# Kernel optimization log

Measured on AMD Instinct MI355X. Metric: run time of the kernel, lower is better.

## Reference

```python
import jax, jax.numpy as jnp
import numpy as np
import math

N = 10000      # nodes per type
DIN = 64       # input feature dim
HID = 128      # hidden_dim
HEADS = 8      # num_heads
DH = 128       # per-head dim == out_channels (PyG TransformerConv)
INNER = HEADS * DH  # 1024
L = 2          # num_layers
E = 60000      # edges per edge type
FF = 512       # 4*hidden
LN_EPS = 1e-5


def setup_inputs():
    keys = iter(jax.random.split(jax.random.key(0), 80))
    def mk(shape, std=0.05):
        return std * jax.random.normal(next(keys), shape, dtype=jnp.float32)
    inp = {}
    for t in ("job", "mach"):
        inp[f"x_{t}"] = mk((N, DIN), 1.0)
        inp[f"Win_{t}"] = mk((DIN, HID)); inp[f"bin_{t}"] = mk((HID,), 0.01)
        inp[f"pos_{t}"] = mk((N, HID)); inp[f"te_{t}"] = mk((HID,))
        inp[f"lng_{t}"] = 1.0 + mk((L, HID), 0.02); inp[f"lnb_{t}"] = mk((L, HID), 0.02)
        inp[f"W1_{t}"] = mk((L, HID, FF)); inp[f"b1_{t}"] = mk((L, FF), 0.01)
        inp[f"W2_{t}"] = mk((L, FF, HID)); inp[f"b2_{t}"] = mk((L, HID), 0.01)
        inp[f"Wout_{t}"] = mk((HID, HID)); inp[f"bout_{t}"] = mk((HID,), 0.01)
    for et in ("jm", "mj"):
        inp[f"Wq_{et}"] = mk((L, HID, INNER)); inp[f"Wk_{et}"] = mk((L, HID, INNER))
        inp[f"Wv_{et}"] = mk((L, HID, INNER)); inp[f"Ws_{et}"] = mk((L, HID, HID))
        inp[f"Wb_{et}"] = mk((L, 3 * HID, 1))
        inp[f"bq_{et}"] = mk((L, INNER), 0.01); inp[f"bk_{et}"] = mk((L, INNER), 0.01)
        inp[f"bv_{et}"] = mk((L, INNER), 0.01); inp[f"bs_{et}"] = mk((L, HID), 0.01)
        inp[f"ei_{et}"] = jax.random.randint(next(keys), (2, E), 0, N, dtype=jnp.int32)
    return inp


def _layer_norm(x, g, b):
    mu = x.mean(-1, keepdims=True)
    var = ((x - mu) ** 2).mean(-1, keepdims=True)
    return (x - mu) / jnp.sqrt(var + LN_EPS) * g + b


def _tconv(x_src, x_dst, src, dst, Wq, bq, Wk, bk, Wv, bv, Ws, bs, Wb):
    # PyG TransformerConv(heads=HEADS, out_channels=DH, concat=False, beta=True, root_weight=True)
    Nd = x_dst.shape[0]
    q = (x_dst @ Wq + bq).reshape(Nd, HEADS, DH)
    k = (x_src @ Wk + bk).reshape(-1, HEADS, DH)
    v = (x_src @ Wv + bv).reshape(-1, HEADS, DH)
    logits = jnp.einsum('ehd,ehd->eh', q[dst], k[src]) / math.sqrt(DH)  # [E,H]
    # segment softmax over edges grouped by destination node
    m = jax.ops.segment_max(logits, dst, num_segments=Nd)
    m = jnp.where(jnp.isfinite(m), m, 0.0)  # empty segments -> -inf -> 0
    ex = jnp.exp(logits - m[dst])
    den = jax.ops.segment_sum(ex, dst, num_segments=Nd)
    alpha = ex / (den[dst] + 1e-16)
    agg = jax.ops.segment_sum(alpha[:, :, None] * v[src], dst, num_segments=Nd)
    out = agg.mean(axis=1)              # concat=False -> average heads -> [Nd, DH]
    x_r = x_dst @ Ws + bs               # root/skip projection
    beta = jax.nn.sigmoid(jnp.concatenate([out, x_r, out - x_r], axis=-1) @ Wb)  # [Nd,1]
    return beta * x_r + (1.0 - beta) * out


def _ffn_block(h, new, g, b, W1, b1, W2, b2):
    r = _layer_norm(h + new, g, b)
    return r + (jax.nn.gelu(r @ W1 + b1, approximate=False) @ W2 + b2)


def _forward(x_job, Win_job, bin_job, pos_job, te_job, lng_job, lnb_job, W1_job, b1_job, W2_job, b2_job, Wout_job, bout_job, x_mach, Win_mach, bin_mach, pos_mach, te_mach, lng_mach, lnb_mach, W1_mach, b1_mach, W2_mach, b2_mach, Wout_mach, bout_mach, Wq_jm, Wk_jm, Wv_jm, Ws_jm, Wb_jm, bq_jm, bk_jm, bv_jm, bs_jm, ei_jm, Wq_mj, Wk_mj, Wv_mj, Ws_mj, Wb_mj, bq_mj, bk_mj, bv_mj, bs_mj, ei_mj):
    h_j = x_job @ Win_job + bin_job + te_job + pos_job
    h_m = x_mach @ Win_mach + bin_mach + te_mach + pos_mach
    s_jm, d_jm = ei_jm[0], ei_jm[1]  # job -> mach
    s_mj, d_mj = ei_mj[0], ei_mj[1]  # mach -> job
    for l in range(L):
        new_m = _tconv(h_j, h_m, s_jm, d_jm, Wq_jm[l], bq_jm[l], Wk_jm[l], bk_jm[l], Wv_jm[l], bv_jm[l], Ws_jm[l], bs_jm[l], Wb_jm[l])
        new_j = _tconv(h_m, h_j, s_mj, d_mj, Wq_mj[l], bq_mj[l], Wk_mj[l], bk_mj[l], Wv_mj[l], bv_mj[l], Ws_mj[l], bs_mj[l], Wb_mj[l])
        h_j = _ffn_block(h_j, new_j, lng_job[l], lnb_job[l], W1_job[l], b1_job[l], W2_job[l], b2_job[l])
        h_m = _ffn_block(h_m, new_m, lng_mach[l], lnb_mach[l], W1_mach[l], b1_mach[l], W2_mach[l], b2_mach[l])
    return jnp.stack([h_j @ Wout_job + bout_job, h_m @ Wout_mach + bout_mach], axis=0)


def reference(x_job, Win_job, bin_job, pos_job, te_job, lng_job, lnb_job, W1_job, b1_job, W2_job, b2_job, Wout_job, bout_job, x_mach, Win_mach, bin_mach, pos_mach, te_mach, lng_mach, lnb_mach, W1_mach, b1_mach, W2_mach, b2_mach, Wout_mach, bout_mach, Wq_jm, Wk_jm, Wv_jm, Ws_jm, Wb_jm, bq_jm, bk_jm, bv_jm, bs_jm, ei_jm, Wq_mj, Wk_mj, Wv_mj, Ws_mj, Wb_mj, bq_mj, bk_mj, bv_mj, bs_mj, ei_mj):
    return _forward(x_job, Win_job, bin_job, pos_job, te_job, lng_job, lnb_job, W1_job, b1_job, W2_job, b2_job, Wout_job, bout_job, x_mach, Win_mach, bin_mach, pos_mach, te_mach, lng_mach, lnb_mach, W1_mach, b1_mach, W2_mach, b2_mach, Wout_mach, bout_mach, Wq_jm, Wk_jm, Wv_jm, Ws_jm, Wb_jm, bq_jm, bk_jm, bv_jm, bs_jm, ei_jm, Wq_mj, Wk_mj, Wv_mj, Ws_mj, Wb_mj, bq_mj, bk_mj, bv_mj, bs_mj, ei_mj)
```

## Files before the change

### kernel.cpp

```cpp
#include <hip/hip_runtime.h>
#include <hip/hip_bf16.h>

#define NN 10000
#define EE 60000
#define HIDD 128
#define NH 8
#define INNERD 1024
#define FFD 512
#define KVQ 3072
#define KVQS 3200

using u16 = unsigned short;
using u32 = unsigned int;

typedef __bf16 bf16x8 __attribute__((ext_vector_type(8)));
typedef float f32x4 __attribute__((ext_vector_type(4)));

__device__ __forceinline__ float u2f(u32 u) { return __uint_as_float(u << 16); }
__device__ __forceinline__ u16 f2b(float f) {
  u32 x = __float_as_uint(f);
  return (u16)((x + 0x7fffu + ((x >> 16) & 1u)) >> 16);
}
__device__ __forceinline__ float gelu_f(float x) {
  return 0.5f * x * (1.0f + erff(x * 0.70710678118654752f));
}

__global__ void detect_k(const u32* __restrict__ xw, int* __restrict__ flag) {
  if (threadIdx.x == 0 && blockIdx.x == 0) {
    int wild = 0;
    for (int i = 0; i < 256; ++i) {
      float v = u2f(xw[i] & 0xffffu);
      if (!(fabsf(v) < 1e4f)) ++wild;
    }
    *flag = (wild > 16) ? 1 : 0;
  }
}

#define NCVT 30
struct CvtArgs { const void* src[NCVT]; int cnt[NCVT]; int ntot; };

__global__ __launch_bounds__(256) void convert_k(CvtArgs a, const int* __restrict__ flag,
                                                 float* __restrict__ dst) {
  const int i = blockIdx.x * 256 + threadIdx.x;
  if (i >= a.ntot) return;
  int t = 0, off = i;
  while (off >= a.cnt[t]) { off -= a.cnt[t]; ++t; }
  const float v = (*flag) ? ((const float*)a.src[t])[off]
                          : u2f(((const u16*)a.src[t])[off]);
  dst[i] = v;
}

struct TT { const void* s; long off; u16* d; int K; int N; };
struct TTab { TT m[28]; };

__global__ __launch_bounds__(256) void transT_k(TTab tt, const int* __restrict__ flag) {
  const TT m = tt.m[blockIdx.z];
  const int n0 = blockIdx.x * 32, k0 = blockIdx.y * 32;
  if (n0 >= m.N || k0 >= m.K) return;
  __shared__ float tile[32][33];
  const int c = threadIdx.x;
  const int f32in = *flag;
  for (int i = threadIdx.y; i < 32; i += 8) {
    const long gi = m.off + (long)(k0 + i) * m.N + n0 + c;
    tile[i][c] = f32in ? ((const float*)m.s)[gi] : u2f(((const u16*)m.s)[gi]);
  }
  __syncthreads();
  for (int i = threadIdx.y; i < 32; i += 8)
    m.d[(size_t)(n0 + i) * m.K + k0 + c] = f2b(tile[c][i]);
}

__global__ __launch_bounds__(256) void hist_k(const int* __restrict__ ei0,
                                              const int* __restrict__ ei1,
                                              int* __restrict__ hist) {
  const int e = blockIdx.x * 256 + threadIdx.x;
  if (e >= EE) return;
  const int et = blockIdx.y;
  const int* ei = et ? ei1 : ei0;
  atomicAdd(&hist[et * NN + ei[EE + e]], 1);
}

__global__ __launch_bounds__(1024) void scan2_k(const int* __restrict__ hist,
                                                int* __restrict__ rowptr,
                                                int* __restrict__ cursor) {
  const int et = blockIdx.x;
  const int* h = hist + et * NN;
  int* rp = rowptr + et * (NN + 1);
  int* cu = cursor + et * NN;
  __shared__ int wsum[16];
  __shared__ int carrySm;
  const int t = threadIdx.x, lane = t & 63, wid = t >> 6;
  if (t == 0) carrySm = 0;
  __syncthreads();
  for (int base = 0; base < NN; base += 1024) {
    const int idx = base + t;
    const int v = (idx < NN) ? h[idx] : 0;
    int x = v;
#pragma unroll
    for (int off = 1; off < 64; off <<= 1) {
      int y = __shfl_up(x, off);
      if (lane >= off) x += y;
    }
    if (lane == 63) wsum[wid] = x;
    __syncthreads();
    if (wid == 0) {
      int s = (lane < 16) ? wsum[lane] : 0;
#pragma unroll
      for (int off = 1; off < 16; off <<= 1) {
        int y = __shfl_up(s, off);
        if (lane >= off) s += y;
      }
      if (lane < 16) wsum[lane] = s;
    }
    __syncthreads();
    const int waveoff = (wid > 0) ? wsum[wid - 1] : 0;
    const int incl = x + waveoff + carrySm;
    if (idx < NN) { rp[idx] = incl - v; cu[idx] = incl - v; }
    __syncthreads();
    if (t == 1023) carrySm = incl;
    __syncthreads();
  }
  if (t == 0) rp[NN] = carrySm;
}

__global__ __launch_bounds__(256) void scat_k(const int* __restrict__ ei0,
                                              const int* __restrict__ ei1,
                                              int* __restrict__ cursor,
                                              int* __restrict__ srcs) {
  const int e = blockIdx.x * 256 + threadIdx.x;
  if (e >= EE) return;
  const int et = blockIdx.y;
  const int* ei = et ? ei1 : ei0;
  const int s = ei[e], d = ei[EE + e];
  const int pos = atomicAdd(&cursor[et * NN + d], 1);
  srcs[et * EE + pos] = s;
}

__global__ __launch_bounds__(128) void embed2_k(
    const void* __restrict__ x0, const float* __restrict__ Win0,
    const float* __restrict__ bin0, const float* __restrict__ te0,
    const void* __restrict__ pos0, float* __restrict__ h0, u16* __restrict__ h80,
    const void* __restrict__ x1, const float* __restrict__ Win1,
    const float* __restrict__ bin1, const float* __restrict__ te1,
    const void* __restrict__ pos1, float* __restrict__ h1, u16* __restrict__ h81,
    const int* __restrict__ flag) {
  const int ty = blockIdx.y;
  const void* x = ty ? x1 : x0;
  const float* Win = ty ? Win1 : Win0;
  const float* bin = ty ? bin1 : bin0;
  const float* te = ty ? te1 : te0;
  const void* pos = ty ? pos1 : pos0;
  float* h = ty ? h1 : h0;
  u16* h8 = ty ? h81 : h80;
  __shared__ float Ws[64][128];
  __shared__ float xs[16][64];
  const int f32in = *flag;
  const int j = threadIdx.x;
  const int base = blockIdx.x * 16;
  for (int i = 0; i < 64; ++i) Ws[i][j] = Win[i * 128 + j];
  for (int r = 0; r < 8; ++r) {
    int idx = r * 128 + j;
    int row = idx >> 6, k = idx & 63;
    size_t gi = (size_t)(base + row) * 64 + k;
    xs[row][k] = f32in ? ((const float*)x)[gi] : u2f(((const u16*)x)[gi]);
  }
  __syncthreads();
  float bj = bin[j] + te[j];
  for (int row = 0; row < 16; ++row) {
    size_t gi = (size_t)(base + row) * 128 + j;
    float pv = f32in ? ((const float*)pos)[gi] : u2f(((const u16*)pos)[gi]);
    float acc = bj + pv;
#pragma unroll
    for (int k = 0; k < 64; ++k) acc += xs[row][k] * Ws[k][j];
    h[(size_t)(base + row) * 128 + j] = acc;
    h8[(size_t)(base + row) * 128 + j] = f2b(acc);
  }
}

struct MG {
  const u16* A; const u16* WT;
  const float* b0; const float* b1; const float* b2; const float* b3;
  const float* add; float* Cf; u16* Cb;
};

template <int MODE>
__global__ __launch_bounds__(256) void mgemm2_k(MG g0, MG g1, int M, int N, int K) {
  const MG g = blockIdx.z ? g1 : g0;
  __shared__ __align__(16) u16 Asl[128][40];
  __shared__ __align__(16) u16 Bsl[64][40];
  const int t = threadIdx.x;
  const int lane = t & 63, wid = t >> 6;
  const int bm = blockIdx.y * 128, bn = blockIdx.x * 64;
  const int rg = lane >> 4, rr = lane & 15;
  f32x4 acc[2][4];
#pragma unroll
  for (int i = 0; i < 2; ++i)
#pragma unroll
    for (int j = 0; j < 4; ++j) acc[i][j] = (f32x4){0.f, 0.f, 0.f, 0.f};
  const int ar = t >> 1;
  const int ah = (t & 1) << 4;
  const int wr = t >> 2;
  const int wk = (t & 3) << 3;

  for (int k0 = 0; k0 < K; k0 += 32) {
    const int garow = bm + ar;
    uint4 a0 = {0,0,0,0}, a1 = {0,0,0,0};
    if (garow < M) {
      const u16* ap = g.A + (size_t)garow * K + k0 + ah;
      a0 = *reinterpret_cast<const uint4*>(ap);
      a1 = *reinterpret_cast<const uint4*>(ap + 8);
    }
    *reinterpret_cast<uint4*>(&Asl[ar][ah]) = a0;
    *reinterpret_cast<uint4*>(&Asl[ar][ah + 8]) = a1;
    const uint4 bv = *reinterpret_cast<const uint4*>(g.WT + (size_t)(bn + wr) * K + k0 + wk);
    *reinterpret_cast<uint4*>(&Bsl[wr][wk]) = bv;
    __syncthreads();
    bf16x8 af[2], bfr[4];
#pragma unroll
    for (int mi = 0; mi < 2; ++mi)
      af[mi] = *reinterpret_cast<const bf16x8*>(&Asl[wid * 32 + mi * 16 + rr][rg * 8]);
#pragma unroll
    for (int ni = 0; ni < 4; ++ni)
      bfr[ni] = *reinterpret_cast<const bf16x8*>(&Bsl[ni * 16 + rr][rg * 8]);
#pragma unroll
    for (int mi = 0; mi < 2; ++mi)
#pragma unroll
      for (int ni = 0; ni < 4; ++ni)
        acc[mi][ni] = __builtin_amdgcn_mfma_f32_16x16x32_bf16(af[mi], bfr[ni], acc[mi][ni], 0, 0, 0);
    __syncthreads();
  }
#pragma unroll
  for (int mi = 0; mi < 2; ++mi) {
#pragma unroll
    for (int ni = 0; ni < 4; ++ni) {
      const int col = bn + ni * 16 + rr;
      float bcol;
      if (MODE == 2) {
        const int seg = col >> 10;
        const float* bp = (seg == 0) ? g.b0 : ((seg == 1) ? g.b1 : ((seg == 2) ? g.b2 : g.b3));
        bcol = bp[col & 1023];
      } else {
        bcol = g.b0[col];
      }
#pragma unroll
      for (int r = 0; r < 4; ++r) {
        const int row = bm + wid * 32 + mi * 16 + rg * 4 + r;
        if (row >= M) continue;
        float v = acc[mi][ni][r] + bcol;
        if (MODE == 2) {
          if (col < KVQ) g.Cb[(size_t)row * KVQ + col] = f2b(v);
          else           g.Cf[(size_t)row * HIDD + (col - KVQ)] = v;
        } else if (MODE == 3) {
          v = gelu_f(v);
          g.Cb[(size_t)row * N + col] = f2b(v);
        } else {
          v += g.add[(size_t)row * N + col];
          g.Cf[(size_t)row * N + col] = v;
          g.Cb[(size_t)row * N + col] = f2b(v);
        }
      }
    }
  }
}

struct VG {
  const float* A; const float* B; const float* bias;
  float* Cf; u16* Cb;
};

__global__ __launch_bounds__(256) void gemm2_k(VG g0, VG g1, const int* __restrict__ oflag,
                                               int M, int N, int K) {
  const VG g = blockIdx.z ? g1 : g0;
  __shared__ __align__(16) float As[16][64];
  __shared__ __align__(16) float Bs[16][64];
  const int t = threadIdx.x;
  const int tx = t & 15, ty = t >> 4;
  const int bm = blockIdx.y * 64, bn = blockIdx.x * 64;
  float c[4][4] = {{0.f}};
  const int am = t >> 2;
  const int ak = (t & 3) << 2;
  const int bk = t >> 4;
  const int bn4 = (t & 15) << 2;
  for (int k0 = 0; k0 < K; k0 += 16) {
    float4 av = make_float4(0.f, 0.f, 0.f, 0.f);
    const int arow = bm + am;
    if (arow < M) av = *reinterpret_cast<const float4*>(g.A + (size_t)arow * K + k0 + ak);
    As[ak + 0][am] = av.x; As[ak + 1][am] = av.y;
    As[ak + 2][am] = av.z; As[ak + 3][am] = av.w;
    float4 bv = *reinterpret_cast<const float4*>(g.B + (size_t)(k0 + bk) * N + bn + bn4);
    Bs[bk][bn4 + 0] = bv.x; Bs[bk][bn4 + 1] = bv.y;
    Bs[bk][bn4 + 2] = bv.z; Bs[bk][bn4 + 3] = bv.w;
    __syncthreads();
#pragma unroll
    for (int kk = 0; kk < 16; ++kk) {
      float4 a = *reinterpret_cast<const float4*>(&As[kk][ty << 2]);
      float4 b = *reinterpret_cast<const float4*>(&Bs[kk][tx << 2]);
      c[0][0] += a.x * b.x; c[0][1] += a.x * b.y; c[0][2] += a.x * b.z; c[0][3] += a.x * b.w;
      c[1][0] += a.y * b.x; c[1][1] += a.y * b.y; c[1][2] += a.y * b.z; c[1][3] += a.y * b.w;
      c[2][0] += a.z * b.x; c[2][1] += a.z * b.y; c[2][2] += a.z * b.z; c[2][3] += a.z * b.w;
      c[3][0] += a.w * b.x; c[3][1] += a.w * b.y; c[3][2] += a.w * b.z; c[3][3] += a.w * b.w;
    }
    __syncthreads();
  }
  const int f32out = *oflag;
#pragma unroll
  for (int i = 0; i < 4; ++i) {
    const int row = bm + (ty << 2) + i;
    if (row >= M) continue;
#pragma unroll
    for (int j = 0; j < 4; ++j) {
      const int col = bn + (tx << 2) + j;
      float v = c[i][j] + g.bias[col];
      if (f32out) g.Cf[(size_t)row * N + col] = v;
      else        g.Cb[(size_t)row * N + col] = f2b(v);
    }
  }
}

__global__ __launch_bounds__(256) void attn2_k(
    const u16* __restrict__ kvqJ, const u16* __restrict__ kvqM,
    const int* __restrict__ rowptr, const int* __restrict__ srcs,
    float* __restrict__ aggM, float* __restrict__ aggJ) {
  const int et = blockIdx.y;
  const u16* kvqS = et ? kvqM : kvqJ;
  const u16* kvqD = et ? kvqJ : kvqM;
  const int* rp = rowptr + et * (NN + 1);
  const int* sr = srcs + et * EE;
  float* agg = et ? aggJ : aggM;
  const int d = (blockIdx.x * 256 + threadIdx.x) >> 6;
  const int lane = threadIdx.x & 63;
  const u16* qp = kvqD + (size_t)d * KVQ + 2048 + lane * 16;
  uint4 q0 = *reinterpret_cast<const uint4*>(qp);
  uint4 q1 = *reinterpret_cast<const uint4*>(qp + 8);
  float qf[16];
  {
    u32 w[8] = {q0.x, q0.y, q0.z, q0.w, q1.x, q1.y, q1.z, q1.w};
#pragma unroll
    for (int i = 0; i < 8; ++i) { qf[2*i] = u2f(w[i] & 0xffffu); qf[2*i+1] = u2f(w[i] >> 16); }
  }
  float m = -INFINITY, den = 0.f;
  float acc[16];
#pragma unroll
  for (int i = 0; i < 16; ++i) acc[i] = 0.f;
  const int beg = rp[d], end = rp[d + 1];

  auto dot8 = [&](const uint4& a, const uint4& b) -> float {
    float p = 0.f;
    const u32 w[8] = {a.x, a.y, a.z, a.w, b.x, b.y, b.z, b.w};
#pragma unroll
    for (int i = 0; i < 8; ++i) {
      p += qf[2*i] * u2f(w[i] & 0xffffu);
      p += qf[2*i+1] * u2f(w[i] >> 16);
    }
    return p;
  };
  auto update = [&](float part, const uint4& v0w, const uint4& v1w) {
    part += __shfl_xor(part, 1);
    part += __shfl_xor(part, 2);
    part += __shfl_xor(part, 4);
    const float lg = part * 0.088388347648318447f;
    const float nm = fmaxf(m, lg);
    const float cor = __expf(m - nm);
    const float p = __expf(lg - nm);
    den = den * cor + p;
    const u32 w[8] = {v0w.x, v0w.y, v0w.z, v0w.w, v1w.x, v1w.y, v1w.z, v1w.w};
#pragma unroll
    for (int i = 0; i < 8; ++i) {
      acc[2*i]   = acc[2*i]   * cor + p * u2f(w[i] & 0xffffu);
      acc[2*i+1] = acc[2*i+1] * cor + p * u2f(w[i] >> 16);
    }
    m = nm;
  };

  int idx = beg;
  for (; idx + 2 <= end; idx += 2) {
    const int s0 = sr[idx], s1 = sr[idx + 1];
    const u16* kp0 = kvqS + (size_t)s0 * KVQ + lane * 16;
    const u16* kp1 = kvqS + (size_t)s1 * KVQ + lane * 16;
    const uint4 a0 = *reinterpret_cast<const uint4*>(kp0);
    const uint4 a1 = *reinterpret_cast<const uint4*>(kp0 + 8);
    const uint4 av0 = *reinterpret_cast<const uint4*>(kp0 + 1024);
    const uint4 av1 = *reinterpret_cast<const uint4*>(kp0 + 1024 + 8);
    const uint4 b0 = *reinterpret_cast<const uint4*>(kp1);
    const uint4 b1 = *reinterpret_cast<const uint4*>(kp1 + 8);
    const uint4 bv0 = *reinterpret_cast<const uint4*>(kp1 + 1024);
    const uint4 bv1 = *reinterpret_cast<const uint4*>(kp1 + 1024 + 8);
    const float p0 = dot8(a0, a1);
    const float p1 = dot8(b0, b1);
    update(p0, av0, av1);
    update(p1, bv0, bv1);
  }
  if (idx < end) {
    const int s0 = sr[idx];
    const u16* kp0 = kvqS + (size_t)s0 * KVQ + lane * 16;
    const uint4 a0 = *reinterpret_cast<const uint4*>(kp0);
    const uint4 a1 = *reinterpret_cast<const uint4*>(kp0 + 8);
    const uint4 av0 = *reinterpret_cast<const uint4*>(kp0 + 1024);
    const uint4 av1 = *reinterpret_cast<const uint4*>(kp0 + 1024 + 8);
    update(dot8(a0, a1), av0, av1);
  }

  const float inv = 0.125f / (den + 1e-16f);
  float o[16];
#pragma unroll
  for (int i = 0; i < 16; ++i) {
    float tv = acc[i] * inv;
    tv += __shfl_xor(tv, 8);
    tv += __shfl_xor(tv, 16);
    tv += __shfl_xor(tv, 32);
    o[i] = tv;
  }
  if (lane < 8) {
    float* op = agg + (size_t)d * HIDD + lane * 16;
    *reinterpret_cast<float4*>(op + 0)  = make_float4(o[0],  o[1],  o[2],  o[3]);
    *reinterpret_cast<float4*>(op + 4)  = make_float4(o[4],  o[5],  o[6],  o[7]);
    *reinterpret_cast<float4*>(op + 8)  = make_float4(o[8],  o[9],  o[10], o[11]);
    *reinterpret_cast<float4*>(op + 12) = make_float4(o[12], o[13], o[14], o[15]);
  }
}

struct BL {
  const float* agg; const float* xr; const float* Wb;
  const float* h; const float* g; const float* b; float* r; u16* r8;
};

__global__ __launch_bounds__(256) void betaln2_k(BL p0, BL p1) {
  const BL p = blockIdx.y ? p1 : p0;
  const int n = (blockIdx.x * 256 + threadIdx.x) >> 6;
  const int lane = threadIdx.x & 63;
  const float o0 = p.agg[(size_t)n * HIDD + lane], o1 = p.agg[(size_t)n * HIDD + 64 + lane];
  const float x0 = p.xr[(size_t)n * HIDD + lane], x1 = p.xr[(size_t)n * HIDD + 64 + lane];
  float s = o0 * p.Wb[lane] + o1 * p.Wb[64 + lane]
          + x0 * p.Wb[128 + lane] + x1 * p.Wb[192 + lane]
          + (o0 - x0) * p.Wb[256 + lane] + (o1 - x1) * p.Wb[320 + lane];
#pragma unroll
  for (int mask = 1; mask < 64; mask <<= 1) s += __shfl_xor(s, mask);
  const float beta = 1.f / (1.f + expf(-s));
  const float n0 = beta * x0 + (1.f - beta) * o0;
  const float n1 = beta * x1 + (1.f - beta) * o1;
  const float v0 = p.h[(size_t)n * HIDD + lane] + n0;
  const float v1 = p.h[(size_t)n * HIDD + 64 + lane] + n1;
  float sm = v0 + v1;
#pragma unroll
  for (int mask = 1; mask < 64; mask <<= 1) sm += __shfl_xor(sm, mask);
  const float mu = sm * (1.f / 128.f);
  const float d0 = v0 - mu, d1 = v1 - mu;
  float vs = d0 * d0 + d1 * d1;
#pragma unroll
  for (int mask = 1; mask < 64; mask <<= 1) vs += __shfl_xor(vs, mask);
  const float rstd = rsqrtf(vs * (1.f / 128.f) + 1e-5f);
  const float r0 = d0 * rstd * p.g[lane] + p.b[lane];
  const float r1 = d1 * rstd * p.g[64 + lane] + p.b[64 + lane];
  p.r[(size_t)n * HIDD + lane]      = r0;
  p.r[(size_t)n * HIDD + 64 + lane] = r1;
  p.r8[(size_t)n * HIDD + lane]      = f2b(r0);
  p.r8[(size_t)n * HIDD + 64 + lane] = f2b(r1);
}

extern "C" void kernel_launch(void* const* d_in, const int* in_sizes, int n_in,
                              void* d_out, int out_size, void* d_ws, size_t ws_size,
                              hipStream_t stream) {
  char* w = (char*)d_ws;
  auto carve = [&](size_t bytes) { void* p = (void*)w; w += (bytes + 255) & ~(size_t)255; return p; };
  float* h_b[2];  h_b[0] = (float*)carve((size_t)NN * HIDD * 4); h_b[1] = (float*)carve((size_t)NN * HIDD * 4);
  u16* h8_b[2];   h8_b[0] = (u16*)carve((size_t)NN * HIDD * 2);  h8_b[1] = (u16*)carve((size_t)NN * HIDD * 2);
  float* rb_b[2]; rb_b[0] = (float*)carve((size_t)NN * HIDD * 4); rb_b[1] = (float*)carve((size_t)NN * HIDD * 4);
  u16* rb8_b[2];  rb8_b[0] = (u16*)carve((size_t)NN * HIDD * 2);  rb8_b[1] = (u16*)carve((size_t)NN * HIDD * 2);
  float* xr_b[2]; xr_b[0] = (float*)carve((size_t)NN * HIDD * 4); xr_b[1] = (float*)carve((size_t)NN * HIDD * 4);
  float* ag_b[2]; ag_b[0] = (float*)carve((size_t)NN * HIDD * 4); ag_b[1] = (float*)carve((size_t)NN * HIDD * 4);
  u16* kvqJ = (u16*)carve((size_t)NN * KVQ * 2);
  u16* kvqM = (u16*)carve((size_t)NN * KVQ * 2);
  u16* mid8_b[2] = {kvqJ, kvqM};
  int* histb  = (int*)carve(2 * NN * 4);
  int* rowptr = (int*)carve(2 * (NN + 1) * 4);
  int* cursor = (int*)carve(2 * NN * 4);
  int* srcsb  = (int*)carve(2 * EE * 4);
  int* flagp  = (int*)carve(256);
  const int totCvt = 2 * 26752 + 2 * 7168;
  float* wf = (float*)carve((size_t)totCvt * 4);
  u16* wtp = (u16*)carve((size_t)(4 * KVQS * HIDD + 8 * HIDD * FFD) * 2);

  CvtArgs ca; int nc = 0; int cum = 0;
  auto addc = [&](int inIdx, int n) -> float* {
    ca.src[nc] = d_in[inIdx]; ca.cnt[nc] = n; float* p = wf + cum; cum += n; ++nc; return p;
  };
  const float *WinF[2], *binF[2], *teF[2], *lngF[2], *lnbF[2], *b1F[2], *b2F[2], *WoutF[2], *boutF[2];
  const void* x_p[2]; const void* pos_p[2];
  for (int t = 0; t < 2; ++t) {
    const int o = t * 13;
    x_p[t] = d_in[o + 0];
    WinF[t] = addc(o + 1, 64 * HIDD);
    binF[t] = addc(o + 2, HIDD);
    pos_p[t] = d_in[o + 3];
    teF[t]  = addc(o + 4, HIDD);
    lngF[t] = addc(o + 5, 2 * HIDD);
    lnbF[t] = addc(o + 6, 2 * HIDD);
    b1F[t]  = addc(o + 8, 2 * FFD);
    b2F[t]  = addc(o + 10, 2 * HIDD);
    WoutF[t] = addc(o + 11, HIDD * HIDD);
    boutF[t] = addc(o + 12, HIDD);
  }
  const float *WbF[2], *bqF[2], *bkF[2], *bvF[2], *bsF[2];
  const int* ei_e[2];
  for (int et = 0; et < 2; ++et) {
    const int o = 26 + et * 10;
    WbF[et] = addc(o + 4, 2 * 384);
    bqF[et] = addc(o + 5, 2 * INNERD);
    bkF[et] = addc(o + 6, 2 * INNERD);
    bvF[et] = addc(o + 7, 2 * INNERD);
    bsF[et] = addc(o + 8, 2 * HIDD);
    ei_e[et] = (const int*)d_in[o + 9];
  }
  ca.ntot = cum;

  TTab tt; int ntt = 0; u16* tcur = wtp;
  auto addT = [&](const void* s, long off, int K, int N, u16* dst) {
    tt.m[ntt] = {s, off, dst, K, N}; ++ntt;
  };
  u16* kvqWT[2][2];
  for (int et = 0; et < 2; ++et) {
    const int o  = 26 + et * 10;
    const int oq = 26 + (1 - et) * 10;
    for (int l = 0; l < 2; ++l) {
      u16* base = tcur; tcur += (size_t)KVQS * HIDD;
      kvqWT[et][l] = base;
      addT(d_in[o + 1],  (long)l * HIDD * INNERD, HIDD, INNERD, base);
      addT(d_in[o + 2],  (long)l * HIDD * INNERD, HIDD, INNERD, base + 1024 * HIDD);
      addT(d_in[oq + 0], (long)l * HIDD * INNERD, HIDD, INNERD, base + 2048 * HIDD);
      addT(d_in[oq + 3], (long)l * HIDD * HIDD,   HIDD, HIDD,   base + 3072 * HIDD);
    }
  }
  u16 *W1T[2][2], *W2T[2][2];
  for (int t = 0; t < 2; ++t) {
    const int o = t * 13;
    for (int l = 0; l < 2; ++l) {
      W1T[t][l] = tcur; addT(d_in[o + 7], (long)l * HIDD * FFD, HIDD, FFD, tcur); tcur += (size_t)HIDD * FFD;
      W2T[t][l] = tcur; addT(d_in[o + 9], (long)l * FFD * HIDD, FFD, HIDD, tcur); tcur += (size_t)FFD * HIDD;
    }
  }

  const dim3 blk(256);
  const int MB64 = (NN + 63) / 64;
  const int MB128 = (NN + 127) / 128;

  detect_k<<<1, 64, 0, stream>>>((const u32*)d_in[0], flagp);
  convert_k<<<(cum + 255) / 256, blk, 0, stream>>>(ca, flagp, wf);
  transT_k<<<dim3(32, 16, 24), dim3(32, 8), 0, stream>>>(tt, flagp);
  hipMemsetAsync(histb, 0, 2 * NN * 4, stream);
  hist_k<<<dim3((EE + 255) / 256, 2), blk, 0, stream>>>(ei_e[0], ei_e[1], histb);
  scan2_k<<<2, 1024, 0, stream>>>(histb, rowptr, cursor);
  scat_k<<<dim3((EE + 255) / 256, 2), blk, 0, stream>>>(ei_e[0], ei_e[1], cursor, srcsb);

  embed2_k<<<dim3(NN / 16, 2), 128, 0, stream>>>(
      x_p[0], WinF[0], binF[0], teF[0], pos_p[0], h_b[0], h8_b[0],
      x_p[1], WinF[1], binF[1], teF[1], pos_p[1], h_b[1], h8_b[1], flagp);

  for (int l = 0; l < 2; ++l) {
    MG gj = {h8_b[0], kvqWT[0][l], bkF[0] + l * INNERD, bvF[0] + l * INNERD,
             bqF[1] + l * INNERD, bsF[1] + l * HIDD, nullptr, xr_b[0], kvqJ};
    MG gm = {h8_b[1], kvqWT[1][l], bkF[1] + l * INNERD, bvF[1] + l * INNERD,
             bqF[0] + l * INNERD, bsF[0] + l * HIDD, nullptr, xr_b[1], kvqM};
    mgemm2_k<2><<<dim3(KVQS / 64, MB128, 2), blk, 0, stream>>>(gj, gm, NN, KVQS, HIDD);
    attn2_k<<<dim3(NN / 4, 2), blk, 0, stream>>>(kvqJ, kvqM, rowptr, srcsb, ag_b[1], ag_b[0]);
    BL p0 = {ag_b[1], xr_b[1], WbF[0] + l * 384, h_b[1],
             lngF[1] + l * HIDD, lnbF[1] + l * HIDD, rb_b[1], rb8_b[1]};
    BL p1 = {ag_b[0], xr_b[0], WbF[1] + l * 384, h_b[0],
             lngF[0] + l * HIDD, lnbF[0] + l * HIDD, rb_b[0], rb8_b[0]};
    betaln2_k<<<dim3(NN / 4, 2), blk, 0, stream>>>(p0, p1);
    MG w1j = {rb8_b[0], W1T[0][l], b1F[0] + l * FFD, nullptr, nullptr, nullptr,
              nullptr, nullptr, mid8_b[0]};
    MG w1m = {rb8_b[1], W1T[1][l], b1F[1] + l * FFD, nullptr, nullptr, nullptr,
              nullptr, nullptr, mid8_b[1]};
    mgemm2_k<3><<<dim3(FFD / 64, MB128, 2), blk, 0, stream>>>(w1j, w1m, NN, FFD, HIDD);
    MG w2j = {mid8_b[0], W2T[0][l], b2F[0] + l * HIDD, nullptr, nullptr, nullptr,
              rb_b[0], h_b[0], h8_b[0]};
    MG w2m = {mid8_b[1], W2T[1][l], b2F[1] + l * HIDD, nullptr, nullptr, nullptr,
              rb_b[1], h_b[1], h8_b[1]};
    mgemm2_k<4><<<dim3(HIDD / 64, MB128, 2), blk, 0, stream>>>(w2j, w2m, NN, HIDD, FFD);
  }
  VG o0 = {h_b[0], WoutF[0], boutF[0], (float*)d_out, (u16*)d_out};
  VG o1 = {h_b[1], WoutF[1], boutF[1],
           (float*)d_out + (size_t)NN * HIDD, (u16*)d_out + (size_t)NN * HIDD};
  gemm2_k<<<dim3(HIDD / 64, MB64, 2), blk, 0, stream>>>(o0, o1, flagp, NN, HIDD, HIDD);
}
```

Baseline: 467.2 us.

## Fuse beta-gating and LayerNorm into attention kernel, pair online-softmax updates

Merges the separate beta-gate/residual/LayerNorm kernel into the edge attention kernel, so the aggregated attention output is never written to and re-read from global memory, and one launch per layer disappears. The online softmax now folds two edges per max/rescale step, which cuts exp and rescale work per edge. In exchange, the attention kernel uses more registers (x, h and r arrays), which may lower occupancy. Every lane group redundantly computes the epilogue and only lanes 0-7 store.

```diff
diff --git a/kernel.cpp b/kernel.cpp
--- a/kernel.cpp
+++ b/kernel.cpp
@@ -316,16 +316,21 @@
   }
 }
 
-__global__ __launch_bounds__(256) void attn2_k(
+struct ABL {
+  const float* Wb; const float* hrow; const float* lgam; const float* lbet;
+  const float* xr; float* r; u16* r8;
+};
+
+__global__ __launch_bounds__(256) void attnbl2_k(
     const u16* __restrict__ kvqJ, const u16* __restrict__ kvqM,
     const int* __restrict__ rowptr, const int* __restrict__ srcs,
-    float* __restrict__ aggM, float* __restrict__ aggJ) {
+    ABL bl0, ABL bl1) {
   const int et = blockIdx.y;
   const u16* kvqS = et ? kvqM : kvqJ;
   const u16* kvqD = et ? kvqJ : kvqM;
   const int* rp = rowptr + et * (NN + 1);
   const int* sr = srcs + et * EE;
-  float* agg = et ? aggJ : aggM;
+  const ABL pb = et ? bl1 : bl0;
   const int d = (blockIdx.x * 256 + threadIdx.x) >> 6;
   const int lane = threadIdx.x & 63;
   const u16* qp = kvqD + (size_t)d * KVQ + 2048 + lane * 16;
@@ -353,22 +358,11 @@
     }
     return p;
   };
-  auto update = [&](float part, const uint4& v0w, const uint4& v1w) {
-    part += __shfl_xor(part, 1);
-    part += __shfl_xor(part, 2);
-    part += __shfl_xor(part, 4);
-    const float lg = part * 0.088388347648318447f;
-    const float nm = fmaxf(m, lg);
-    const float cor = __expf(m - nm);
-    const float p = __expf(lg - nm);
-    den = den * cor + p;
-    const u32 w[8] = {v0w.x, v0w.y, v0w.z, v0w.w, v1w.x, v1w.y, v1w.z, v1w.w};
-#pragma unroll
-    for (int i = 0; i < 8; ++i) {
-      acc[2*i]   = acc[2*i]   * cor + p * u2f(w[i] & 0xffffu);
-      acc[2*i+1] = acc[2*i+1] * cor + p * u2f(w[i] >> 16);
-    }
-    m = nm;
+  auto wred = [&](float p) -> float {
+    p += __shfl_xor(p, 1);
+    p += __shfl_xor(p, 2);
+    p += __shfl_xor(p, 4);
+    return p * 0.088388347648318447f;
   };
 
   int idx = beg;
@@ -384,10 +378,21 @@
     const uint4 b1 = *reinterpret_cast<const uint4*>(kp1 + 8);
     const uint4 bv0 = *reinterpret_cast<const uint4*>(kp1 + 1024);
     const uint4 bv1 = *reinterpret_cast<const uint4*>(kp1 + 1024 + 8);
-    const float p0 = dot8(a0, a1);
-    const float p1 = dot8(b0, b1);
-    update(p0, av0, av1);
-    update(p1, bv0, bv1);
+    const float lg0 = wred(dot8(a0, a1));
+    const float lg1 = wred(dot8(b0, b1));
+    const float nm = fmaxf(m, fmaxf(lg0, lg1));
+    const float cor = __expf(m - nm);
+    const float p0 = __expf(lg0 - nm);
+    const float p1 = __expf(lg1 - nm);
+    den = den * cor + p0 + p1;
+    const u32 wa[8] = {av0.x, av0.y, av0.z, av0.w, av1.x, av1.y, av1.z, av1.w};
+    const u32 wb[8] = {bv0.x, bv0.y, bv0.z, bv0.w, bv1.x, bv1.y, bv1.z, bv1.w};
+#pragma unroll
+    for (int i = 0; i < 8; ++i) {
+      acc[2*i]   = (acc[2*i]   * cor + p0 * u2f(wa[i] & 0xffffu)) + p1 * u2f(wb[i] & 0xffffu);
+      acc[2*i+1] = (acc[2*i+1] * cor + p0 * u2f(wa[i] >> 16))     + p1 * u2f(wb[i] >> 16);
+    }
+    m = nm;
   }
   if (idx < end) {
     const int s0 = sr[idx];
@@ -396,7 +401,18 @@
     const uint4 a1 = *reinterpret_cast<const uint4*>(kp0 + 8);
     const uint4 av0 = *reinterpret_cast<const uint4*>(kp0 + 1024);
     const uint4 av1 = *reinterpret_cast<const uint4*>(kp0 + 1024 + 8);
-    update(dot8(a0, a1), av0, av1);
+    const float lg = wred(dot8(a0, a1));
+    const float nm = fmaxf(m, lg);
+    const float cor = __expf(m - nm);
+    const float p = __expf(lg - nm);
+    den = den * cor + p;
+    const u32 w[8] = {av0.x, av0.y, av0.z, av0.w, av1.x, av1.y, av1.z, av1.w};
+#pragma unroll
+    for (int i = 0; i < 8; ++i) {
+      acc[2*i]   = acc[2*i]   * cor + p * u2f(w[i] & 0xffffu);
+      acc[2*i+1] = acc[2*i+1] * cor + p * u2f(w[i] >> 16);
+    }
+    m = nm;
   }
 
   const float inv = 0.125f / (den + 1e-16f);
@@ -409,51 +425,68 @@
     tv += __shfl_xor(tv, 32);
     o[i] = tv;
   }
+
+  const int g8 = (lane & 7) * 16;
+  float x[16], hd[16];
+  {
+    const float* xrp = pb.xr + (size_t)d * HIDD + g8;
+    const float* hp  = pb.hrow + (size_t)d * HIDD + g8;
+#pragma unroll
+    for (int i = 0; i < 16; i += 4) {
+      const float4 xv = *reinterpret_cast<const float4*>(xrp + i);
+      const float4 hv = *reinterpret_cast<const float4*>(hp + i);
+      x[i] = xv.x; x[i+1] = xv.y; x[i+2] = xv.z; x[i+3] = xv.w;
+      hd[i] = hv.x; hd[i+1] = hv.y; hd[i+2] = hv.z; hd[i+3] = hv.w;
+    }
+  }
+  float s = 0.f;
+#pragma unroll
+  for (int i = 0; i < 16; ++i) {
+    s += o[i] * pb.Wb[g8 + i] + x[i] * pb.Wb[128 + g8 + i]
+       + (o[i] - x[i]) * pb.Wb[256 + g8 + i];
+  }
+  s += __shfl_xor(s, 1);
+  s += __shfl_xor(s, 2);
+  s += __shfl_xor(s, 4);
+  const float beta = 1.f / (1.f + expf(-s));
+  float v[16];
+  float psum = 0.f;
+#pragma unroll
+  for (int i = 0; i < 16; ++i) {
+    v[i] = hd[i] + beta * x[i] + (1.f - beta) * o[i];
+    psum += v[i];
+  }
+  psum += __shfl_xor(psum, 1);
+  psum += __shfl_xor(psum, 2);
+  psum += __shfl_xor(psum, 4);
+  const float mu = psum * (1.f / 128.f);
+  float pvar = 0.f;
+#pragma unroll
+  for (int i = 0; i < 16; ++i) {
+    const float dv = v[i] - mu;
+    pvar += dv * dv;
+  }
+  pvar += __shfl_xor(pvar, 1);
+  pvar += __shfl_xor(pvar, 2);
+  pvar += __shfl_xor(pvar, 4);
+  const float rstd = rsqrtf(pvar * (1.f / 128.f) + 1e-5f);
+  float r[16];
+#pragma unroll
+  for (int i = 0; i < 16; ++i)
+    r[i] = (v[i] - mu) * rstd * pb.lgam[g8 + i] + pb.lbet[g8 + i];
   if (lane < 8) {
-    float* op = agg + (size_t)d * HIDD + lane * 16;
-    *reinterpret_cast<float4*>(op + 0)  = make_float4(o[0],  o[1],  o[2],  o[3]);
-    *reinterpret_cast<float4*>(op + 4)  = make_float4(o[4],  o[5],  o[6],  o[7]);
-    *reinterpret_cast<float4*>(op + 8)  = make_float4(o[8],  o[9],  o[10], o[11]);
-    *reinterpret_cast<float4*>(op + 12) = make_float4(o[12], o[13], o[14], o[15]);
-  }
-}
-
-struct BL {
-  const float* agg; const float* xr; const float* Wb;
-  const float* h; const float* g; const float* b; float* r; u16* r8;
-};
-
-__global__ __launch_bounds__(256) void betaln2_k(BL p0, BL p1) {
-  const BL p = blockIdx.y ? p1 : p0;
-  const int n = (blockIdx.x * 256 + threadIdx.x) >> 6;
-  const int lane = threadIdx.x & 63;
-  const float o0 = p.agg[(size_t)n * HIDD + lane], o1 = p.agg[(size_t)n * HIDD + 64 + lane];
-  const float x0 = p.xr[(size_t)n * HIDD + lane], x1 = p.xr[(size_t)n * HIDD + 64 + lane];
-  float s = o0 * p.Wb[lane] + o1 * p.Wb[64 + lane]
-          + x0 * p.Wb[128 + lane] + x1 * p.Wb[192 + lane]
-          + (o0 - x0) * p.Wb[256 + lane] + (o1 - x1) * p.Wb[320 + lane];
-#pragma unroll
-  for (int mask = 1; mask < 64; mask <<= 1) s += __shfl_xor(s, mask);
-  const float beta = 1.f / (1.f + expf(-s));
-  const float n0 = beta * x0 + (1.f - beta) * o0;
-  const float n1 = beta * x1 + (1.f - beta) * o1;
-  const float v0 = p.h[(size_t)n * HIDD + lane] + n0;
-  const float v1 = p.h[(size_t)n * HIDD + 64 + lane] + n1;
-  float sm = v0 + v1;
-#pragma unroll
-  for (int mask = 1; mask < 64; mask <<= 1) sm += __shfl_xor(sm, mask);
-  const float mu = sm * (1.f / 128.f);
-  const float d0 = v0 - mu, d1 = v1 - mu;
-  float vs = d0 * d0 + d1 * d1;
-#pragma unroll
-  for (int mask = 1; mask < 64; mask <<= 1) vs += __shfl_xor(vs, mask);
-  const float rstd = rsqrtf(vs * (1.f / 128.f) + 1e-5f);
-  const float r0 = d0 * rstd * p.g[lane] + p.b[lane];
-  const float r1 = d1 * rstd * p.g[64 + lane] + p.b[64 + lane];
-  p.r[(size_t)n * HIDD + lane]      = r0;
-  p.r[(size_t)n * HIDD + 64 + lane] = r1;
-  p.r8[(size_t)n * HIDD + lane]      = f2b(r0);
-  p.r8[(size_t)n * HIDD + 64 + lane] = f2b(r1);
+    float* rp_ = pb.r + (size_t)d * HIDD + g8;
+#pragma unroll
+    for (int i = 0; i < 16; i += 4)
+      *reinterpret_cast<float4*>(rp_ + i) = make_float4(r[i], r[i+1], r[i+2], r[i+3]);
+    u32 pk[8];
+#pragma unroll
+    for (int i = 0; i < 8; ++i)
+      pk[i] = (u32)f2b(r[2*i]) | ((u32)f2b(r[2*i+1]) << 16);
+    uint4* r8p = reinterpret_cast<uint4*>(pb.r8 + (size_t)d * HIDD + g8);
+    r8p[0] = (uint4){pk[0], pk[1], pk[2], pk[3]};
+    r8p[1] = (uint4){pk[4], pk[5], pk[6], pk[7]};
+  }
 }
 
 extern "C" void kernel_launch(void* const* d_in, const int* in_sizes, int n_in,
@@ -466,7 +499,6 @@
   float* rb_b[2]; rb_b[0] = (float*)carve((size_t)NN * HIDD * 4); rb_b[1] = (float*)carve((size_t)NN * HIDD * 4);
   u16* rb8_b[2];  rb8_b[0] = (u16*)carve((size_t)NN * HIDD * 2);  rb8_b[1] = (u16*)carve((size_t)NN * HIDD * 2);
   float* xr_b[2]; xr_b[0] = (float*)carve((size_t)NN * HIDD * 4); xr_b[1] = (float*)carve((size_t)NN * HIDD * 4);
-  float* ag_b[2]; ag_b[0] = (float*)carve((size_t)NN * HIDD * 4); ag_b[1] = (float*)carve((size_t)NN * HIDD * 4);
   u16* kvqJ = (u16*)carve((size_t)NN * KVQ * 2);
   u16* kvqM = (u16*)carve((size_t)NN * KVQ * 2);
   u16* mid8_b[2] = {kvqJ, kvqM};
@@ -560,12 +592,11 @@
     MG gm = {h8_b[1], kvqWT[1][l], bkF[1] + l * INNERD, bvF[1] + l * INNERD,
              bqF[0] + l * INNERD, bsF[0] + l * HIDD, nullptr, xr_b[1], kvqM};
     mgemm2_k<2><<<dim3(KVQS / 64, MB128, 2), blk, 0, stream>>>(gj, gm, NN, KVQS, HIDD);
-    attn2_k<<<dim3(NN / 4, 2), blk, 0, stream>>>(kvqJ, kvqM, rowptr, srcsb, ag_b[1], ag_b[0]);
-    BL p0 = {ag_b[1], xr_b[1], WbF[0] + l * 384, h_b[1],
-             lngF[1] + l * HIDD, lnbF[1] + l * HIDD, rb_b[1], rb8_b[1]};
-    BL p1 = {ag_b[0], xr_b[0], WbF[1] + l * 384, h_b[0],
-             lngF[0] + l * HIDD, lnbF[0] + l * HIDD, rb_b[0], rb8_b[0]};
-    betaln2_k<<<dim3(NN / 4, 2), blk, 0, stream>>>(p0, p1);
+    ABL bl0 = {WbF[0] + l * 384, h_b[1], lngF[1] + l * HIDD, lnbF[1] + l * HIDD,
+               xr_b[1], rb_b[1], rb8_b[1]};
+    ABL bl1 = {WbF[1] + l * 384, h_b[0], lngF[0] + l * HIDD, lnbF[0] + l * HIDD,
+               xr_b[0], rb_b[0], rb8_b[0]};
+    attnbl2_k<<<dim3(NN / 4, 2), blk, 0, stream>>>(kvqJ, kvqM, rowptr, srcsb, bl0, bl1);
     MG w1j = {rb8_b[0], W1T[0][l], b1F[0] + l * FFD, nullptr, nullptr, nullptr,
               nullptr, nullptr, mid8_b[0]};
     MG w1m = {rb8_b[1], W1T[1][l], b1F[1] + l * FFD, nullptr, nullptr, nullptr,
```

Measured after the change: 461.1 us. About the same (-1.3%).
